# Kernel tuning notes

Hardware: AMD Instinct MI355X
Metric: run time of the kernel (lower is better)

Reference implementation:

```python
import jax, jax.numpy as jnp
import numpy as np

B, T, D = 2, 2048, 1024
H, HS = 16, 64  # n_head, head_size; H*HS == D
THETA = 10000.0


def setup_inputs() -> dict:
    key = jax.random.key(0)
    ks = jax.random.split(key, 10)
    s = 0.02
    return {
        "x": jax.random.normal(ks[0], (B, T, D), jnp.float32),
        "attention_mask": jnp.ones((B, T), jnp.int32),
        # weights stored [in, out] (transposed torch Linear weight)
        "Wq": jax.random.normal(ks[1], (D, H * HS), jnp.float32) * s,
        "bq": jax.random.normal(ks[2], (H * HS,), jnp.float32) * s,
        "Wk": jax.random.normal(ks[3], (D, H * HS), jnp.float32) * s,
        "bk": jax.random.normal(ks[4], (H * HS,), jnp.float32) * s,
        "Wv": jax.random.normal(ks[5], (D, H * HS), jnp.float32) * s,
        "bv": jax.random.normal(ks[6], (H * HS,), jnp.float32) * s,
        "Wo": jax.random.normal(ks[7], (H * HS, D), jnp.float32) * s,
        "bo": jax.random.normal(ks[8], (D,), jnp.float32) * s,
    }


def _rotate_half(x):
    x1, x2 = x[..., : HS // 2], x[..., HS // 2:]
    return jnp.concatenate((-x2, x1), axis=-1)


def _rope_tables(seq_len, dtype):
    inv_freq = 1.0 / (THETA ** (jnp.arange(0, HS, 2, dtype=jnp.float32) / HS))
    t = jnp.arange(seq_len, dtype=jnp.float32)
    freqs = t[:, None] * inv_freq[None, :]            # [T, HS/2]
    emb = jnp.concatenate((freqs, freqs), axis=-1)    # [T, HS]
    return jnp.cos(emb).astype(dtype), jnp.sin(emb).astype(dtype)


def attention_fwd(x, attention_mask, Wq, bq, Wk, bk, Wv, bv, Wo, bo):
    b, t, c = x.shape
    # QKV projections -> [B, H, T, HS]
    q = (x @ Wq + bq).reshape(b, t, H, HS).transpose(0, 2, 1, 3)
    k = (x @ Wk + bk).reshape(b, t, H, HS).transpose(0, 2, 1, 3)
    v = (x @ Wv + bv).reshape(b, t, H, HS).transpose(0, 2, 1, 3)
    # rotary embedding
    cos, sin = _rope_tables(t, x.dtype)               # [T, HS]
    q = q * cos + _rotate_half(q) * sin
    k = k * cos + _rotate_half(k) * sin
    # expanded causal+padding mask: mask[:,None,None,:] expanded to [B,1,T,T] then tril
    causal = jnp.tril(jnp.ones((t, t), dtype=bool))
    keep = (attention_mask[:, None, None, :] != 0) & causal[None, None]  # [B,1,T,T]
    scale = 1.0 / np.sqrt(HS)
    scores = jnp.einsum('bhqd,bhkd->bhqk', q, k) * scale
    scores = jnp.where(keep, scores, jnp.finfo(scores.dtype).min)
    att = jax.nn.softmax(scores, axis=-1)
    y = jnp.einsum('bhqk,bhkd->bhqd', att, v)         # [B,H,T,HS]
    y = y.transpose(0, 2, 1, 3).reshape(b, t, H * HS)
    return y @ Wo + bo


def reference(x, attention_mask, Wq, bq, Wk, bk, Wv, bv, Wo, bo):
    return attention_fwd(x, attention_mask, Wq, bq, Wk, bk, Wv, bv, Wo, bo)
```

## Files before the change

kernel.cpp:

```cpp
#include <hip/hip_runtime.h>

#define T_SEQ 2048
#define NB 2
#define NH 16
#define HS 64
#define DMODEL 1024
#define NEG_BIG (-3.0e38f)
#define FIXED_M 16.0f

typedef __attribute__((ext_vector_type(8))) short bf16x8;
typedef __attribute__((ext_vector_type(4))) float f32x4;
#define MFMA16 __builtin_amdgcn_mfma_f32_16x16x32_bf16

__device__ __forceinline__ float bfu2f(unsigned int u) {
    union { unsigned int i; float f; } z; z.i = u << 16; return z.f;
}
__device__ __forceinline__ unsigned short f2bfu(float f) {
    union { float f; unsigned int i; } z; z.f = f;
    unsigned int x = z.i;
    unsigned int r = x + 0x7fffu + ((x >> 16) & 1u);
    return (unsigned short)(r >> 16);
}
__device__ __forceinline__ unsigned int pack_bf16(float a, float b) {
    union { float f; unsigned int u; } x, y; x.f = a; y.f = b;
    return __builtin_amdgcn_perm(y.u + 0x8000u, x.u + 0x8000u, 0x07060302u);
}
__device__ __forceinline__ void gl2lds16(const unsigned short* g, unsigned short* l) {
    __builtin_amdgcn_global_load_lds(
        (const __attribute__((address_space(1))) unsigned int*)g,
        (__attribute__((address_space(3))) unsigned int*)l, 16, 0, 0);
}

__global__ __launch_bounds__(256) void prep_kernel(
    const float4* __restrict__ x4, ushort4* __restrict__ o4,
    const float* __restrict__ W0, const float* __restrict__ W1,
    const float* __restrict__ W2, const float* __restrict__ W3,
    unsigned short* __restrict__ T0, unsigned short* __restrict__ T1,
    unsigned short* __restrict__ T2, unsigned short* __restrict__ T3)
{
    const int t = threadIdx.x;
    if (blockIdx.z < 4) {
        __shared__ float tile[32][33];
        const float* W = (blockIdx.z == 0) ? W0 : (blockIdx.z == 1) ? W1 : (blockIdx.z == 2) ? W2 : W3;
        unsigned short* T = (blockIdx.z == 0) ? T0 : (blockIdx.z == 1) ? T1 : (blockIdx.z == 2) ? T2 : T3;
        const int k0 = blockIdx.x * 32, n0 = blockIdx.y * 32;
        const int r = t >> 5, c = t & 31;
        #pragma unroll
        for (int i = 0; i < 4; ++i)
            tile[r + 8 * i][c] = W[(size_t)(k0 + r + 8 * i) * DMODEL + n0 + c];
        __syncthreads();
        #pragma unroll
        for (int i = 0; i < 4; ++i)
            T[(size_t)(n0 + r + 8 * i) * DMODEL + k0 + c] = f2bfu(tile[c][r + 8 * i]);
    } else {
        const int n4 = NB * T_SEQ * DMODEL / 4;
        for (int i = (blockIdx.y * 32 + blockIdx.x) * 256 + t; i < n4; i += 32 * 32 * 256) {
            float4 f = x4[i];
            ushort4 u;
            u.x = f2bfu(f.x); u.y = f2bfu(f.y); u.z = f2bfu(f.z); u.w = f2bfu(f.w);
            o4[i] = u;
        }
    }
}

__global__ __launch_bounds__(256) void qkv_mfma_kernel(
    const unsigned short* __restrict__ A,
    const unsigned short* __restrict__ Wqt, const unsigned short* __restrict__ Wkt,
    const unsigned short* __restrict__ Wvt,
    const float* __restrict__ bq, const float* __restrict__ bk, const float* __restrict__ bv,
    unsigned short* __restrict__ qo, unsigned short* __restrict__ ko,
    unsigned short* __restrict__ vt)
{
    __shared__ unsigned short As[128 * 64];
    __shared__ unsigned short Bs[128 * 64];
    const int tid = threadIdx.x;
    const int wave = tid >> 6, lane = tid & 63;
    const int lane15 = lane & 15, quad = lane >> 4;
    const int sw = lane15 & 7;
    const int z = blockIdx.z;
    const unsigned short* Bt = (z == 0) ? Wqt : (z == 1) ? Wkt : Wvt;
    const float* bias = (z == 0) ? bq : (z == 1) ? bk : bv;
    const int m0 = blockIdx.x * 128, n0 = blockIdx.y * 128;
    const int mh = (wave & 1) * 64, nh = (wave >> 1) * 64;
    const int oks0 = ((0 + quad) ^ sw) * 8;
    const int oks1 = ((4 + quad) ^ sw) * 8;

    f32x4 acc[4][4];
    #pragma unroll
    for (int i = 0; i < 4; ++i)
        #pragma unroll
        for (int j = 0; j < 4; ++j) acc[i][j] = (f32x4){0.f, 0.f, 0.f, 0.f};

    int srow[4], soff[4];
    #pragma unroll
    for (int it = 0; it < 4; ++it) {
        int cc = it * 256 + tid;
        srow[it] = cc >> 3;
        soff[it] = ((cc & 7) ^ (srow[it] & 7)) * 8;
    }

    for (int kk = 0; kk < 16; ++kk) {
        __syncthreads();
        #pragma unroll
        for (int it = 0; it < 4; ++it) {
            int cc = it * 256 + tid;
            gl2lds16(A  + (size_t)(m0 + srow[it]) * DMODEL + kk * 64 + soff[it], As + cc * 8);
            gl2lds16(Bt + (size_t)(n0 + srow[it]) * DMODEL + kk * 64 + soff[it], Bs + cc * 8);
        }
        __syncthreads();
        #pragma unroll
        for (int ks = 0; ks < 2; ++ks) {
            const int o = ks ? oks1 : oks0;
            bf16x8 af[4], bfr[4];
            #pragma unroll
            for (int i = 0; i < 4; ++i)
                af[i] = *(const bf16x8*)(As + (mh + i * 16 + lane15) * 64 + o);
            #pragma unroll
            for (int j = 0; j < 4; ++j)
                bfr[j] = *(const bf16x8*)(Bs + (nh + j * 16 + lane15) * 64 + o);
            #pragma unroll
            for (int i = 0; i < 4; ++i)
                #pragma unroll
                for (int j = 0; j < 4; ++j)
                    acc[i][j] = MFMA16(af[i], bfr[j], acc[i][j], 0, 0, 0);
        }
    }

    const int n0c = n0 + nh;
    const int head = n0c >> 6;
    const float bj0 = bias[n0c + lane15];
    const float bj1 = bias[n0c + 16 + lane15];
    const float bj2 = bias[n0c + 32 + lane15];
    const float bj3 = bias[n0c + 48 + lane15];

    if (z < 2) {
        unsigned short* outp = (z == 0) ? qo : ko;
        const float osc = (z == 0) ? 0.18033688011112042f : 1.0f;
        const float inv0 = __builtin_exp2f(-(float)(lane15)      * 0.41524101186092029f);
        const float inv1 = __builtin_exp2f(-(float)(lane15 + 16) * 0.41524101186092029f);
        #pragma unroll
        for (int i = 0; i < 4; ++i) {
            #pragma unroll
            for (int r = 0; r < 4; ++r) {
                int tok = m0 + mh + i * 16 + quad * 4 + r;
                int bb = tok >> 11, t = tok & (T_SEQ - 1);
                float a0 = (float)t * inv0, a1 = (float)t * inv1;
                float sn0, cs0, sn1, cs1;
                __sincosf(a0, &sn0, &cs0);
                __sincosf(a1, &sn1, &cs1);
                float v0 = acc[i][0][r] + bj0, v1 = acc[i][1][r] + bj1;
                float v2 = acc[i][2][r] + bj2, v3 = acc[i][3][r] + bj3;
                size_t base = ((size_t)(bb * NH + head) * T_SEQ + t) * HS;
                outp[base + lane15]      = f2bfu((v0 * cs0 - v2 * sn0) * osc);
                outp[base + 16 + lane15] = f2bfu((v1 * cs1 - v3 * sn1) * osc);
                outp[base + 32 + lane15] = f2bfu((v2 * cs0 + v0 * sn0) * osc);
                outp[base + 48 + lane15] = f2bfu((v3 * cs1 + v1 * sn1) * osc);
            }
        }
    } else {
        #pragma unroll
        for (int i = 0; i < 4; ++i) {
            int tok0_ = m0 + mh + i * 16 + quad * 4;
            int bb = tok0_ >> 11, t0 = tok0_ & (T_SEQ - 1);
            #pragma unroll
            for (int j = 0; j < 4; ++j) {
                float bj = (j == 0) ? bj0 : (j == 1) ? bj1 : (j == 2) ? bj2 : bj3;
                ushort4 u;
                u.x = f2bfu(acc[i][j][0] + bj);
                u.y = f2bfu(acc[i][j][1] + bj);
                u.z = f2bfu(acc[i][j][2] + bj);
                u.w = f2bfu(acc[i][j][3] + bj);
                *(ushort4*)(vt + ((size_t)(bb * NH + head) * HS + j * 16 + lane15) * T_SEQ + t0) = u;
            }
        }
    }
}

__global__ __launch_bounds__(128, 2) void attn_mfma_kernel(
    const unsigned short* __restrict__ q,
    const unsigned short* __restrict__ k,
    const unsigned short* __restrict__ vt,
    const int* __restrict__ mask,
    unsigned short* __restrict__ pO,
    float* __restrict__ pl)
{
    __shared__ unsigned short Ks[64 * 64];
    __shared__ unsigned short Vs[64 * 64];
    __shared__ unsigned short Pt[2][32 * 72];
    const int tid = threadIdx.x;
    const int wave = tid >> 6, lane = tid & 63;
    const int lane15 = lane & 15, quad = lane >> 4;
    const int sw = lane15 & 7;
    const int oks0 = ((0 + quad) ^ sw) * 8;
    const int oks1 = ((4 + quad) ^ sw) * 8;
    const int bid = blockIdx.x;
    const int bh = bid & 31;
    const int cid = 47 - (bid >> 5);
    int qB, c;
    if (cid < 16) { qB = cid; c = 0; }
    else { int t = cid - 16; qB = 16 + (t >> 1); c = t & 1; }
    const int slot = bh * 48 + ((qB < 16) ? qB : 16 + ((qB - 16) << 1)) + c;
    const int b = bh >> 4;
    const int q0 = qB * 64 + wave * 32;
    const int kt0 = c * 16, kt1 = (kt0 + 15 < qB) ? kt0 + 15 : qB;

    const unsigned short* kbase = k  + (size_t)bh * T_SEQ * HS;
    const unsigned short* vbase = vt + (size_t)bh * HS * T_SEQ;

    bf16x8 qf[2][2];
    #pragma unroll
    for (int g = 0; g < 2; ++g) {
        const unsigned short* qrow = q + ((size_t)bh * T_SEQ + q0 + g * 16 + lane15) * HS;
        qf[g][0] = *(const bf16x8*)(qrow + quad * 8);
        qf[g][1] = *(const bf16x8*)(qrow + 32 + quad * 8);
    }

    f32x4 accO[2][4];
    #pragma unroll
    for (int g = 0; g < 2; ++g)
        #pragma unroll
        for (int dt = 0; dt < 4; ++dt) accO[g][dt] = (f32x4){0.f, 0.f, 0.f, 0.f};
    float l_part[2] = {0.f, 0.f};

    int srow[4], soff[4];
    #pragma unroll
    for (int it = 0; it < 4; ++it) {
        int cc = it * 128 + tid;
        srow[it] = cc >> 3;
        soff[it] = ((cc & 7) ^ (srow[it] & 7)) * 8;
    }

    for (int kt = kt0; kt <= kt1; ++kt) {
        const int k0 = kt * 64;
        __syncthreads();
        #pragma unroll
        for (int it = 0; it < 4; ++it) {
            int cc = it * 128 + tid;
            gl2lds16(kbase + (size_t)(k0 + srow[it]) * HS + soff[it], Ks + cc * 8);
            gl2lds16(vbase + (size_t)srow[it] * T_SEQ + k0 + soff[it], Vs + cc * 8);
        }
        unsigned long long bal = __ballot(mask[b * T_SEQ + k0 + lane] != 0);
        __syncthreads();

        f32x4 s[2][4];
        #pragma unroll
        for (int jt = 0; jt < 4; ++jt) {
            bf16x8 kf0 = *(const bf16x8*)(Ks + (jt * 16 + lane15) * 64 + oks0);
            bf16x8 kf1 = *(const bf16x8*)(Ks + (jt * 16 + lane15) * 64 + oks1);
            #pragma unroll
            for (int g = 0; g < 2; ++g) {
                f32x4 t_ = (f32x4){0.f, 0.f, 0.f, 0.f};
                t_ = MFMA16(kf0, qf[g][0], t_, 0, 0, 0);
                t_ = MFMA16(kf1, qf[g][1], t_, 0, 0, 0);
                s[g][jt] = t_;
            }
        }

        const bool need_mask = (k0 + 63 > q0) || (bal != ~0ull);
        if (need_mask) {
            #pragma unroll
            for (int g = 0; g < 2; ++g) {
                const int qpos = q0 + g * 16 + lane15;
                #pragma unroll
                for (int jt = 0; jt < 4; ++jt) {
                    unsigned int mnib = (unsigned int)(bal >> (jt * 16 + quad * 4)) & 15u;
                    #pragma unroll
                    for (int r = 0; r < 4; ++r) {
                        int kpos = k0 + jt * 16 + quad * 4 + r;
                        bool ok = (kpos <= qpos) && ((mnib >> r) & 1u);
                        s[g][jt][r] = ok ? s[g][jt][r] : NEG_BIG;
                    }
                }
            }
        }
        #pragma unroll
        for (int g = 0; g < 2; ++g)
            #pragma unroll
            for (int jt = 0; jt < 4; ++jt)
                #pragma unroll
                for (int r = 0; r < 4; ++r) {
                    float p = exp2f(s[g][jt][r] - FIXED_M);
                    s[g][jt][r] = p;
                    l_part[g] += p;
                }

        #pragma unroll
        for (int g = 0; g < 2; ++g)
            #pragma unroll
            for (int jt = 0; jt < 4; ++jt) {
                unsigned int p01 = pack_bf16(s[g][jt][0], s[g][jt][1]);
                unsigned int p23 = pack_bf16(s[g][jt][2], s[g][jt][3]);
                *(uint2*)(&Pt[wave][(g * 16 + lane15) * 72 + jt * 16 + quad * 4]) = make_uint2(p01, p23);
            }

        bf16x8 pf[2][2];
        #pragma unroll
        for (int g = 0; g < 2; ++g) {
            pf[g][0] = *(const bf16x8*)(&Pt[wave][(g * 16 + lane15) * 72 + quad * 8]);
            pf[g][1] = *(const bf16x8*)(&Pt[wave][(g * 16 + lane15) * 72 + 32 + quad * 8]);
        }
        #pragma unroll
        for (int dt = 0; dt < 4; ++dt) {
            bf16x8 vf0 = *(const bf16x8*)(Vs + (dt * 16 + lane15) * 64 + oks0);
            bf16x8 vf1 = *(const bf16x8*)(Vs + (dt * 16 + lane15) * 64 + oks1);
            #pragma unroll
            for (int g = 0; g < 2; ++g) {
                accO[g][dt] = MFMA16(pf[g][0], vf0, accO[g][dt], 0, 0, 0);
                accO[g][dt] = MFMA16(pf[g][1], vf1, accO[g][dt], 0, 0, 0);
            }
        }
    }

    unsigned short* ob = pO + (size_t)slot * 4096;
    #pragma unroll
    for (int g = 0; g < 2; ++g)
        #pragma unroll
        for (int r = 0; r < 4; ++r) {
            int row = wave * 32 + g * 16 + quad * 4 + r;
            #pragma unroll
            for (int dt = 0; dt < 4; ++dt)
                ob[row * 64 + dt * 16 + lane15] = f2bfu(accO[g][dt][r]);
        }
    #pragma unroll
    for (int g = 0; g < 2; ++g) {
        float l = l_part[g];
        l += __shfl_xor(l, 16);
        l += __shfl_xor(l, 32);
        if (quad == 0)
            pl[slot * 64 + wave * 32 + g * 16 + lane15] = l;
    }
}

__global__ __launch_bounds__(256) void attn_combine_kernel(
    const unsigned short* __restrict__ pO, const float* __restrict__ pl,
    unsigned short* __restrict__ y)
{
    const int qB = blockIdx.x, bh = blockIdx.y;
    const int b = bh >> 4, h = bh & 15;
    const int tid = threadIdx.x;
    const int row = tid >> 2, cb = (tid & 3) * 16;
    const int nch = (qB < 16) ? 1 : 2;
    const int slot0 = bh * 48 + ((qB < 16) ? qB : 16 + ((qB - 16) << 1));
    float L = pl[slot0 * 64 + row];
    if (nch == 2) L += pl[(slot0 + 1) * 64 + row];
    const float invL = 1.0f / L;
    const unsigned short* o0 = pO + (size_t)slot0 * 4096 + row * 64 + cb;
    const unsigned short* o1 = o0 + 4096;
    unsigned short* yrow = y + (size_t)(b * T_SEQ + qB * 64 + row) * DMODEL + h * HS + cb;
    #pragma unroll
    for (int j = 0; j < 4; ++j) {
        ushort4 u0 = *(const ushort4*)(o0 + j * 4);
        float a0 = bfu2f(u0.x), a1 = bfu2f(u0.y), a2 = bfu2f(u0.z), a3 = bfu2f(u0.w);
        if (nch == 2) {
            ushort4 u1 = *(const ushort4*)(o1 + j * 4);
            a0 += bfu2f(u1.x); a1 += bfu2f(u1.y); a2 += bfu2f(u1.z); a3 += bfu2f(u1.w);
        }
        ushort4 o;
        o.x = f2bfu(a0 * invL); o.y = f2bfu(a1 * invL);
        o.z = f2bfu(a2 * invL); o.w = f2bfu(a3 * invL);
        *(ushort4*)(yrow + j * 4) = o;
    }
}

__global__ __launch_bounds__(256) void outproj_mfma_kernel(
    const unsigned short* __restrict__ A,
    const unsigned short* __restrict__ Bt,
    const float* __restrict__ bo, float* __restrict__ out)
{
    __shared__ unsigned short As[64 * 64];
    __shared__ unsigned short Bs[128 * 64];
    const int tid = threadIdx.x;
    const int wave = tid >> 6, lane = tid & 63;
    const int lane15 = lane & 15, quad = lane >> 4;
    const int sw = lane15 & 7;
    const int oks0 = ((0 + quad) ^ sw) * 8;
    const int oks1 = ((4 + quad) ^ sw) * 8;
    const int m0 = blockIdx.x * 64, n0 = blockIdx.y * 128;
    const int mh = (wave & 1) * 32, nh = (wave >> 1) * 64;

    f32x4 acc[2][4];
    #pragma unroll
    for (int i = 0; i < 2; ++i)
        #pragma unroll
        for (int j = 0; j < 4; ++j) acc[i][j] = (f32x4){0.f, 0.f, 0.f, 0.f};

    int srow[4], soff[4];
    #pragma unroll
    for (int it = 0; it < 4; ++it) {
        int cc = it * 256 + tid;
        srow[it] = cc >> 3;
        soff[it] = ((cc & 7) ^ (srow[it] & 7)) * 8;
    }

    for (int kk = 0; kk < 16; ++kk) {
        __syncthreads();
        #pragma unroll
        for (int it = 0; it < 2; ++it) {
            int cc = it * 256 + tid;
            gl2lds16(A + (size_t)(m0 + srow[it]) * DMODEL + kk * 64 + soff[it], As + cc * 8);
        }
        #pragma unroll
        for (int it = 0; it < 4; ++it) {
            int cc = it * 256 + tid;
            gl2lds16(Bt + (size_t)(n0 + srow[it]) * DMODEL + kk * 64 + soff[it], Bs + cc * 8);
        }
        __syncthreads();
        #pragma unroll
        for (int ks = 0; ks < 2; ++ks) {
            const int o = ks ? oks1 : oks0;
            bf16x8 af[2], bfr[4];
            #pragma unroll
            for (int i = 0; i < 2; ++i)
                af[i] = *(const bf16x8*)(As + (mh + i * 16 + lane15) * 64 + o);
            #pragma unroll
            for (int j = 0; j < 4; ++j)
                bfr[j] = *(const bf16x8*)(Bs + (nh + j * 16 + lane15) * 64 + o);
            #pragma unroll
            for (int i = 0; i < 2; ++i)
                #pragma unroll
                for (int j = 0; j < 4; ++j)
                    acc[i][j] = MFMA16(af[i], bfr[j], acc[i][j], 0, 0, 0);
        }
    }

    const int n0c = n0 + nh;
    const float bj0 = bo[n0c + lane15];
    const float bj1 = bo[n0c + 16 + lane15];
    const float bj2 = bo[n0c + 32 + lane15];
    const float bj3 = bo[n0c + 48 + lane15];
    #pragma unroll
    for (int i = 0; i < 2; ++i) {
        #pragma unroll
        for (int r = 0; r < 4; ++r) {
            int tok = m0 + mh + i * 16 + quad * 4 + r;
            float* orow = out + (size_t)tok * DMODEL + n0c;
            orow[lane15]      = acc[i][0][r] + bj0;
            orow[16 + lane15] = acc[i][1][r] + bj1;
            orow[32 + lane15] = acc[i][2][r] + bj2;
            orow[48 + lane15] = acc[i][3][r] + bj3;
        }
    }
}

extern "C" void kernel_launch(void* const* d_in, const int* in_sizes, int n_in,
                              void* d_out, int out_size, void* d_ws, size_t ws_size,
                              hipStream_t stream)
{
    const float* x  = (const float*)d_in[0];
    const int* mask = (const int*)d_in[1];
    const float* Wq = (const float*)d_in[2];
    const float* bq = (const float*)d_in[3];
    const float* Wk = (const float*)d_in[4];
    const float* bk = (const float*)d_in[5];
    const float* Wv = (const float*)d_in[6];
    const float* bv = (const float*)d_in[7];
    const float* Wo = (const float*)d_in[8];
    const float* bo = (const float*)d_in[9];

    unsigned short* ws = (unsigned short*)d_ws;
    const size_t M1 = 1024 * 1024;
    unsigned short* xb  = ws;
    unsigned short* Wqt = ws + 4 * M1;
    unsigned short* Wkt = ws + 5 * M1;
    unsigned short* Wvt = ws + 6 * M1;
    unsigned short* Wot = ws + 7 * M1;
    unsigned short* qw  = ws + 8 * M1;
    unsigned short* kw  = ws + 12 * M1;
    unsigned short* vtw = ws + 16 * M1;
    unsigned short* yw  = ws + 20 * M1;
    unsigned short* pO  = ws + 24 * M1;
    float* pl = (float*)(ws + 30 * M1);

    prep_kernel<<<dim3(32, 32, 5), 256, 0, stream>>>(
        (const float4*)x, (ushort4*)xb, Wq, Wk, Wv, Wo, Wqt, Wkt, Wvt, Wot);
    qkv_mfma_kernel<<<dim3(32, 8, 3), 256, 0, stream>>>(
        xb, Wqt, Wkt, Wvt, bq, bk, bv, qw, kw, vtw);
    attn_mfma_kernel<<<1536, 128, 0, stream>>>(
        qw, kw, vtw, mask, pO, pl);
    attn_combine_kernel<<<dim3(32, 32), 256, 0, stream>>>(
        pO, pl, yw);
    outproj_mfma_kernel<<<dim3(64, 8), 256, 0, stream>>>(
        yw, Wot, bo, (float*)d_out);
}
```

Baseline: 206.4 us.

## Split causal attention KV range into more balanced chunks and swizzle P tile

Query blocks are now split into 1 to 4 KV chunks depending on their position, so the attention grid grows from 1536 to 2560 blocks with more even per-block work. The combine kernel is generalized to sum a variable number of partial outputs. The P staging buffer drops its padding and uses the same XOR swizzle as K and V to avoid LDS bank conflicts. The workspace is rearranged so pO overlaps the xb and weight buffers, which are dead by the time attention runs. In exchange the split adds more partial-output traffic and combine work.

```diff
diff --git a/kernel.cpp b/kernel.cpp
--- a/kernel.cpp
+++ b/kernel.cpp
@@ -186,7 +186,7 @@
 {
     __shared__ unsigned short Ks[64 * 64];
     __shared__ unsigned short Vs[64 * 64];
-    __shared__ unsigned short Pt[2][32 * 72];
+    __shared__ unsigned short Pt[2][32 * 64];
     const int tid = threadIdx.x;
     const int wave = tid >> 6, lane = tid & 63;
     const int lane15 = lane & 15, quad = lane >> 4;
@@ -195,14 +195,19 @@
     const int oks1 = ((4 + quad) ^ sw) * 8;
     const int bid = blockIdx.x;
     const int bh = bid & 31;
-    const int cid = 47 - (bid >> 5);
+    const int u = 79 - (bid >> 5);
     int qB, c;
-    if (cid < 16) { qB = cid; c = 0; }
-    else { int t = cid - 16; qB = 16 + (t >> 1); c = t & 1; }
-    const int slot = bh * 48 + ((qB < 16) ? qB : 16 + ((qB - 16) << 1)) + c;
+    if (u < 8)       { qB = u;                 c = 0; }
+    else if (u < 24) { int t = u - 8;  qB = 8  + (t >> 1); c = t & 1; }
+    else if (u < 48) { int t = u - 24; qB = 16 + t / 3;    c = t % 3; }
+    else             { int t = u - 48; qB = 24 + (t >> 2); c = t & 3; }
+    const int slot = bh * 80 + u;
+    const int nc  = (qB + 8) >> 3;
+    const int len = (qB + nc) / nc;
+    const int kt0 = c * len;
+    const int kt1 = (kt0 + len - 1 < qB) ? kt0 + len - 1 : qB;
     const int b = bh >> 4;
     const int q0 = qB * 64 + wave * 32;
-    const int kt0 = c * 16, kt1 = (kt0 + 15 < qB) ? kt0 + 15 : qB;
 
     const unsigned short* kbase = k  + (size_t)bh * T_SEQ * HS;
     const unsigned short* vbase = vt + (size_t)bh * HS * T_SEQ;
@@ -290,14 +295,16 @@
             for (int jt = 0; jt < 4; ++jt) {
                 unsigned int p01 = pack_bf16(s[g][jt][0], s[g][jt][1]);
                 unsigned int p23 = pack_bf16(s[g][jt][2], s[g][jt][3]);
-                *(uint2*)(&Pt[wave][(g * 16 + lane15) * 72 + jt * 16 + quad * 4]) = make_uint2(p01, p23);
+                int pchunk = (2 * jt + (quad >> 1)) ^ sw;
+                int paddr = (g * 16 + lane15) * 64 + pchunk * 8 + (quad & 1) * 4;
+                *(uint2*)(&Pt[wave][paddr]) = make_uint2(p01, p23);
             }
 
         bf16x8 pf[2][2];
         #pragma unroll
         for (int g = 0; g < 2; ++g) {
-            pf[g][0] = *(const bf16x8*)(&Pt[wave][(g * 16 + lane15) * 72 + quad * 8]);
-            pf[g][1] = *(const bf16x8*)(&Pt[wave][(g * 16 + lane15) * 72 + 32 + quad * 8]);
+            pf[g][0] = *(const bf16x8*)(&Pt[wave][(g * 16 + lane15) * 64 + oks0]);
+            pf[g][1] = *(const bf16x8*)(&Pt[wave][(g * 16 + lane15) * 64 + oks1]);
         }
         #pragma unroll
         for (int dt = 0; dt < 4; ++dt) {
@@ -339,25 +346,33 @@
     const int b = bh >> 4, h = bh & 15;
     const int tid = threadIdx.x;
     const int row = tid >> 2, cb = (tid & 3) * 16;
-    const int nch = (qB < 16) ? 1 : 2;
-    const int slot0 = bh * 48 + ((qB < 16) ? qB : 16 + ((qB - 16) << 1));
-    float L = pl[slot0 * 64 + row];
-    if (nch == 2) L += pl[(slot0 + 1) * 64 + row];
+    const int nch = (qB + 8) >> 3;
+    const int p = (qB < 8) ? qB : (qB < 16) ? 8 + 2 * (qB - 8)
+               : (qB < 24) ? 24 + 3 * (qB - 16) : 48 + 4 * (qB - 24);
+    const int slot0 = bh * 80 + p;
+
+    float L = 0.f;
+    for (int ch = 0; ch < nch; ++ch) L += pl[(slot0 + ch) * 64 + row];
     const float invL = 1.0f / L;
-    const unsigned short* o0 = pO + (size_t)slot0 * 4096 + row * 64 + cb;
-    const unsigned short* o1 = o0 + 4096;
+
+    float a[16];
+    #pragma unroll
+    for (int i = 0; i < 16; ++i) a[i] = 0.f;
+    for (int ch = 0; ch < nch; ++ch) {
+        const unsigned short* o = pO + (size_t)(slot0 + ch) * 4096 + row * 64 + cb;
+        #pragma unroll
+        for (int j = 0; j < 4; ++j) {
+            ushort4 u = *(const ushort4*)(o + j * 4);
+            a[j * 4 + 0] += bfu2f(u.x); a[j * 4 + 1] += bfu2f(u.y);
+            a[j * 4 + 2] += bfu2f(u.z); a[j * 4 + 3] += bfu2f(u.w);
+        }
+    }
     unsigned short* yrow = y + (size_t)(b * T_SEQ + qB * 64 + row) * DMODEL + h * HS + cb;
     #pragma unroll
     for (int j = 0; j < 4; ++j) {
-        ushort4 u0 = *(const ushort4*)(o0 + j * 4);
-        float a0 = bfu2f(u0.x), a1 = bfu2f(u0.y), a2 = bfu2f(u0.z), a3 = bfu2f(u0.w);
-        if (nch == 2) {
-            ushort4 u1 = *(const ushort4*)(o1 + j * 4);
-            a0 += bfu2f(u1.x); a1 += bfu2f(u1.y); a2 += bfu2f(u1.z); a3 += bfu2f(u1.w);
-        }
         ushort4 o;
-        o.x = f2bfu(a0 * invL); o.y = f2bfu(a1 * invL);
-        o.z = f2bfu(a2 * invL); o.w = f2bfu(a3 * invL);
+        o.x = f2bfu(a[j * 4 + 0] * invL); o.y = f2bfu(a[j * 4 + 1] * invL);
+        o.z = f2bfu(a[j * 4 + 2] * invL); o.w = f2bfu(a[j * 4 + 3] * invL);
         *(ushort4*)(yrow + j * 4) = o;
     }
 }
@@ -459,23 +474,23 @@
 
     unsigned short* ws = (unsigned short*)d_ws;
     const size_t M1 = 1024 * 1024;
-    unsigned short* xb  = ws;
-    unsigned short* Wqt = ws + 4 * M1;
-    unsigned short* Wkt = ws + 5 * M1;
-    unsigned short* Wvt = ws + 6 * M1;
-    unsigned short* Wot = ws + 7 * M1;
-    unsigned short* qw  = ws + 8 * M1;
-    unsigned short* kw  = ws + 12 * M1;
-    unsigned short* vtw = ws + 16 * M1;
-    unsigned short* yw  = ws + 20 * M1;
-    unsigned short* pO  = ws + 24 * M1;
-    float* pl = (float*)(ws + 30 * M1);
+    unsigned short* qw  = ws;
+    unsigned short* kw  = ws + 4 * M1;
+    unsigned short* vtw = ws + 8 * M1;
+    unsigned short* yw  = ws + 12 * M1;
+    unsigned short* Wot = ws + 16 * M1;
+    unsigned short* xb  = ws + 17 * M1;
+    unsigned short* Wqt = ws + 21 * M1;
+    unsigned short* Wkt = ws + 22 * M1;
+    unsigned short* Wvt = ws + 23 * M1;
+    unsigned short* pO  = ws + 17 * M1;
+    float* pl = (float*)(ws + 27 * M1);
 
     prep_kernel<<<dim3(32, 32, 5), 256, 0, stream>>>(
         (const float4*)x, (ushort4*)xb, Wq, Wk, Wv, Wo, Wqt, Wkt, Wvt, Wot);
     qkv_mfma_kernel<<<dim3(32, 8, 3), 256, 0, stream>>>(
         xb, Wqt, Wkt, Wvt, bq, bk, bv, qw, kw, vtw);
-    attn_mfma_kernel<<<1536, 128, 0, stream>>>(
+    attn_mfma_kernel<<<2560, 128, 0, stream>>>(
         qw, kw, vtw, mask, pO, pl);
     attn_combine_kernel<<<dim3(32, 32), 256, 0, stream>>>(
         pO, pl, yw);
```

New measurement: 198.8 us. 3.7% less time.
